# Kernel tuning notes

Hardware: AMD Instinct MI355X
Metric: run time of the kernel (lower is better)

## Reference

```python
import jax, jax.numpy as jnp
import numpy as np

NUM_POINTS = 4_000_000
RADIUS = 2.5
IMG = 1024


def setup_inputs() -> dict:
    key = jax.random.key(0)
    k1, k2, k3, k4 = jax.random.split(key, 4)
    # Uniform sampling inside a sphere, mirroring the torch __init__
    phi = jax.random.uniform(k1, (NUM_POINTS,)) * 2 * np.pi
    costheta = jax.random.uniform(k2, (NUM_POINTS,)) * 2 - 1
    u = jax.random.uniform(k3, (NUM_POINTS,))
    theta = jnp.arccos(costheta)
    r = RADIUS * u ** (1.0 / 3.0)
    x = r * jnp.sin(theta) * jnp.cos(phi)
    y = r * jnp.sin(theta) * jnp.sin(phi)
    z = r * jnp.cos(theta)
    positions = jnp.stack([x, y, z], axis=-1).astype(jnp.float32)  # [N,3]
    colors = jax.random.uniform(k4, (NUM_POINTS, 3), dtype=jnp.float32)
    # Camera at origin looking down +z, points translated to z in [2.5, 7.5]
    camera_pose = jnp.eye(4, dtype=jnp.float32).at[2, 3].set(5.0)
    intrinsics = jnp.array([[800.0, 0.0, 512.0],
                            [0.0, 800.0, 512.0],
                            [0.0, 0.0, 1.0]], dtype=jnp.float32)
    return {"positions": positions, "colors": colors,
            "camera_pose": camera_pose, "intrinsics": intrinsics,
            "H": IMG, "W": IMG}


def reference(positions, colors, camera_pose, intrinsics, H, W):
    # points_cam = (R @ P^T)^T + t^T
    R = camera_pose[:3, :3]
    t = camera_pose[:3, 3]
    pc = positions @ R.T + t  # [N,3]
    x, y, z = pc[:, 0], pc[:, 1], pc[:, 2]
    fx, fy = intrinsics[0, 0], intrinsics[1, 1]
    cx, cy = intrinsics[0, 2], intrinsics[1, 2]
    u = fx * x / z + cx
    v = fy * y / z + cy
    # int() truncation toward zero, matching the torch loop
    xi = u.astype(jnp.int32)
    yi = v.astype(jnp.int32)
    valid = (xi >= 0) & (xi < W) & (yi >= 0) & (yi < H)
    n = positions.shape[0]
    pix = jnp.where(valid, yi * W + xi, H * W)  # invalid -> sentinel segment
    winner = jax.ops.segment_max(jnp.arange(n, dtype=jnp.int32), pix,
                                 num_segments=H * W + 1)[: H * W]
    has = winner >= 0  # empty segments get iinfo(int32).min
    img_flat = jnp.where(has[:, None],
                         colors[jnp.clip(winner, 0, n - 1)],
                         jnp.float32(0.0))  # [H*W, 3]
    img = img_flat.reshape(H, W, 3).transpose(2, 0, 1)[None]  # [1,3,H,W]
    return jnp.clip(img, 0.0, 1.0)
```

## Files before the change

### kernel.cpp

```cpp
#include <hip/hip_runtime.h>


#define NB      1024
#define TB      512
#define TBP     1024
#define NT      1024
#define GP      4
#define NG      (NT / GP)
#define PPB_MAX 4096
#define IMGW    1024
#define IMGHW   (1024 * 1024)

__host__ __device__ __forceinline__ unsigned align8u(unsigned x) {
    return (x + 7u) & ~7u;
}

__global__ void __launch_bounds__(TB)
binsort_kernel(const float* __restrict__ pos,
               const float* __restrict__ pose,
               const float* __restrict__ intr,
               unsigned* __restrict__ bins,
               unsigned* __restrict__ histG,
               int n, int ppb, int region) {
    __shared__ unsigned stash[PPB_MAX];
    __shared__ unsigned h[NT];
    __shared__ unsigned base_[NT];
    __shared__ unsigned cur[NT];
    __shared__ unsigned sc[TB];

    int tid = threadIdx.x;
    for (int t = tid; t < NT; t += TB) h[t] = 0;
    __syncthreads();

    float r00 = pose[0], r01 = pose[1], r02 = pose[2],  t0 = pose[3];
    float r10 = pose[4], r11 = pose[5], r12 = pose[6],  t1 = pose[7];
    float r20 = pose[8], r21 = pose[9], r22 = pose[10], t2 = pose[11];
    float fx = intr[0], cx = intr[2];
    float fy = intr[4], cy = intr[5];

    int start = blockIdx.x * ppb;
    int cnt = min(start + ppb, n) - start;
    if (cnt < 0) cnt = 0;

    const float4* p4 = (const float4*)(pos + (size_t)3 * (size_t)start);
    for (int j4 = tid * 4; j4 < cnt; j4 += TB * 4) {
        int g = j4 >> 2;
        float4 A = p4[3 * g + 0];
        float4 B = p4[3 * g + 1];
        float4 C = p4[3 * g + 2];
        float xs0 = A.x, ys0 = A.y, zs0 = A.z;
        float xs1 = A.w, ys1 = B.x, zs1 = B.y;
        float xs2 = B.z, ys2 = B.w, zs2 = C.x;
        float xs3 = C.y, ys3 = C.z, zs3 = C.w;

        unsigned pv[4];
        #define PROJ(K, PX, PY, PZ)                                          \
        {                                                                    \
            float x = r00 * PX + r01 * PY + r02 * PZ + t0;                   \
            float y = r10 * PX + r11 * PY + r12 * PZ + t1;                   \
            float z = r20 * PX + r21 * PY + r22 * PZ + t2;                   \
            float u = fx * x / z + cx;                                       \
            float v = fy * y / z + cy;                                       \
            int xi = (int)u;                                                 \
            int yi = (int)v;                                                 \
            unsigned p = 0xFFFFFFFFu;                                        \
            if (xi >= 0 && xi < IMGW && yi >= 0 && yi < IMGW) {              \
                p = ((unsigned)yi << 10) | (unsigned)xi;                     \
                int tt = ((yi >> 5) << 5) + (xi >> 5);                       \
                atomicAdd(&h[tt], 1u);                                       \
            }                                                                \
            pv[K] = p;                                                       \
        }
        PROJ(0, xs0, ys0, zs0)
        PROJ(1, xs1, ys1, zs1)
        PROJ(2, xs2, ys2, zs2)
        PROJ(3, xs3, ys3, zs3)
        #undef PROJ

        *(uint4*)&stash[j4] = make_uint4(pv[0], pv[1], pv[2], pv[3]);
    }
    __syncthreads();

    unsigned c0 = h[2 * tid];
    unsigned c1 = h[2 * tid + 1];
    unsigned v = c0 + c1;
    sc[tid] = v;
    __syncthreads();
    for (int off = 1; off < TB; off <<= 1) {
        unsigned add = (tid >= off) ? sc[tid - off] : 0u;
        __syncthreads();
        v += add;
        sc[tid] = v;
        __syncthreads();
    }
    base_[2 * tid]     = v - c0 - c1;
    base_[2 * tid + 1] = v - c1;
    __syncthreads();

    for (int t = tid; t < NT; t += TB) {
        cur[t] = base_[t];
        histG[(size_t)(t >> 2) * (NB * 4) + (blockIdx.x << 2) + (t & 3)] =
            (base_[t] << 16) | h[t];
    }
    __syncthreads();

    unsigned* myRegion = bins + (size_t)blockIdx.x * (size_t)region;
    for (int j = tid; j < cnt; j += TB) {
        unsigned pv = stash[j];
        if (pv == 0xFFFFFFFFu) continue;
        unsigned xi = pv & 1023u, yi = pv >> 10;
        unsigned t  = ((yi >> 5) << 5) + (xi >> 5);
        unsigned lp = ((yi & 31u) << 5) + (xi & 31u);
        unsigned slot = atomicAdd(&cur[t], 1u);
        myRegion[slot] = (lp << 22) | (unsigned)(start + j);
    }
}

__global__ void __launch_bounds__(TBP)
paint_kernel(const unsigned* __restrict__ bins,
             const unsigned* __restrict__ histG,
             const float* __restrict__ colors,
             float* __restrict__ out,
             int region) {
    __shared__ uint4    hgs[NB];
    __shared__ unsigned win[GP * 1024];
    int g = blockIdx.x;
    int tid = threadIdx.x;

    hgs[tid] = ((const uint4*)histG)[((size_t)g << 10) + tid];
    #pragma unroll
    for (int l = tid; l < GP * 1024; l += TBP) win[l] = 0;
    __syncthreads();

    int grp = tid >> 4, lane16 = tid & 15;
    for (int b = grp; b < NB; b += (TBP / 16)) {
        uint4 pk = hgs[b];
        unsigned c0 = pk.x & 0xFFFFu, c1 = pk.y & 0xFFFFu;
        unsigned c2 = pk.z & 0xFFFFu, c3 = pk.w & 0xFFFFu;
        unsigned b01 = c0 + c1, b012 = b01 + c2;
        unsigned total = b012 + c3;
        const unsigned* p = bins + (size_t)b * (size_t)region + (pk.x >> 16);
        for (unsigned k = lane16; k < total; k += 16) {
            unsigned e = p[k];
            unsigned s = (k >= c0) + (k >= b01) + (k >= b012);
            atomicMax(&win[(s << 10) + (e >> 22)], (e & 0x3FFFFFu) + 1u);
        }
    }
    __syncthreads();

    int tx0 = ((g * GP) & 31) << 5;
    int ty0 = ((g * GP) >> 5) << 5;
    for (int l = tid; l < GP * 1024; l += TBP) {
        int lx = l & 127, ly = l >> 7;
        int s = lx >> 5, col = lx & 31;
        unsigned w = win[(s << 10) + (ly << 5) + col];
        float r = 0.0f, gc = 0.0f, bl = 0.0f;
        if (w) {
            unsigned wi = w - 1u;
            r  = fminf(fmaxf(colors[3 * wi + 0], 0.0f), 1.0f);
            gc = fminf(fmaxf(colors[3 * wi + 1], 0.0f), 1.0f);
            bl = fminf(fmaxf(colors[3 * wi + 2], 0.0f), 1.0f);
        }
        int p = (ty0 + ly) * IMGW + tx0 + lx;
        out[p] = r;
        out[IMGHW + p] = gc;
        out[2 * IMGHW + p] = bl;
    }
}


__global__ void proj_simple(const float* __restrict__ pos,
                            const float* __restrict__ pose,
                            const float* __restrict__ intr,
                            const int* __restrict__ Hp,
                            const int* __restrict__ Wp,
                            int* __restrict__ winner, int n) {
    int i = blockIdx.x * blockDim.x + threadIdx.x;
    if (i >= n) return;
    float px = pos[3 * i], py = pos[3 * i + 1], pz = pos[3 * i + 2];
    float x = pose[0] * px + pose[1] * py + pose[2]  * pz + pose[3];
    float y = pose[4] * px + pose[5] * py + pose[6]  * pz + pose[7];
    float z = pose[8] * px + pose[9] * py + pose[10] * pz + pose[11];
    float u = intr[0] * x / z + intr[2];
    float v = intr[4] * y / z + intr[5];
    int xi = (int)u, yi = (int)v;
    int W = *Wp, H = *Hp;
    if (xi >= 0 && xi < W && yi >= 0 && yi < H) atomicMax(&winner[yi * W + xi], i);
}

__global__ void paint_simple(const int* __restrict__ winner,
                             const float* __restrict__ colors,
                             float* __restrict__ out, int HW) {
    int p = blockIdx.x * blockDim.x + threadIdx.x;
    if (p >= HW) return;
    int w = winner[p];
    float r = 0.0f, g = 0.0f, b = 0.0f;
    if (w >= 0) {
        r = fminf(fmaxf(colors[3 * w + 0], 0.0f), 1.0f);
        g = fminf(fmaxf(colors[3 * w + 1], 0.0f), 1.0f);
        b = fminf(fmaxf(colors[3 * w + 2], 0.0f), 1.0f);
    }
    out[p] = r; out[HW + p] = g; out[2 * HW + p] = b;
}

extern "C" void kernel_launch(void* const* d_in, const int* in_sizes, int n_in,
                              void* d_out, int out_size, void* d_ws, size_t ws_size,
                              hipStream_t stream) {
    const float* positions = (const float*)d_in[0];
    const float* colors    = (const float*)d_in[1];
    const float* pose      = (const float*)d_in[2];
    const float* intr      = (const float*)d_in[3];
    const int*   Hp        = (const int*)d_in[4];
    const int*   Wp        = (const int*)d_in[5];
    float* out = (float*)d_out;

    int n  = in_sizes[0] / 3;
    int HW = out_size / 3;

    int ppb = ((n + NB - 1) / NB + 3) & ~3;
    int region = (int)align8u((unsigned)ppb);
    unsigned* bins  = (unsigned*)d_ws;
    unsigned* histG = bins + (size_t)NB * (size_t)region;
    size_t needFast = ((size_t)NB * region + (size_t)NB * NT) * sizeof(unsigned);

    bool fast = (HW == IMGHW) && (n >= 4096) && ((n & 3) == 0) &&
                (ppb <= PPB_MAX) && (n <= 4000000) && (ws_size >= needFast);

    if (fast) {
        binsort_kernel<<<NB, TB, 0, stream>>>(positions, pose, intr,
                                              bins, histG, n, ppb, region);
        paint_kernel<<<NG, TBP, 0, stream>>>(bins, histG, colors, out, region);
        return;
    }

    int* winner = (int*)d_ws;
    const int block = 256;
    hipMemsetAsync(winner, 0xFF, (size_t)HW * sizeof(int), stream);
    int grid = (n + block - 1) / block;
    proj_simple<<<grid, block, 0, stream>>>(positions, pose, intr, Hp, Wp,
                                            winner, n);
    int grid2 = (HW + block - 1) / block;
    paint_simple<<<grid2, block, 0, stream>>>(winner, colors, out, HW);
}
```

Baseline: 64.66 us.

## Split paint pass across source-bin slices and add merge-gather kernel

The paint kernel is split so each of the 256 pixel groups is handled by 4 blocks, each covering a quarter of the source bins. Each block writes its partial per-pixel winner indices to a workspace buffer. A new merge kernel takes the max across the 4 partials and gathers the colors. The aim is to raise parallelism from 256 large blocks to 1024 smaller ones so the paint phase fills the GPU better, at the cost of an extra 16 MB partial write and read plus one more kernel launch.

```diff
diff --git a/kernel.cpp b/kernel.cpp
--- a/kernel.cpp
+++ b/kernel.cpp
@@ -3,10 +3,11 @@
 
 #define NB      1024
 #define TB      512
-#define TBP     1024
 #define NT      1024
 #define GP      4
 #define NG      (NT / GP)
+#define RS      4
+#define TPP     256
 #define PPB_MAX 4096
 #define IMGW    1024
 #define IMGHW   (1024 * 1024)
@@ -116,56 +117,69 @@
     }
 }
 
-__global__ void __launch_bounds__(TBP)
-paint_kernel(const unsigned* __restrict__ bins,
-             const unsigned* __restrict__ histG,
-             const float* __restrict__ colors,
-             float* __restrict__ out,
-             int region) {
-    __shared__ uint4    hgs[NB];
+__global__ void __launch_bounds__(TPP)
+paint_partial_kernel(const unsigned* __restrict__ bins,
+                     const unsigned* __restrict__ histG,
+                     unsigned* __restrict__ winpart,
+                     int region) {
+    __shared__ uint4    hgs[NB / RS];
     __shared__ unsigned win[GP * 1024];
-    int g = blockIdx.x;
+    int g = blockIdx.x & (NG - 1);
+    int s = blockIdx.x >> 8;
     int tid = threadIdx.x;
 
-    hgs[tid] = ((const uint4*)histG)[((size_t)g << 10) + tid];
+    hgs[tid] = ((const uint4*)histG)[((size_t)g << 10) + (s << 8) + tid];
     #pragma unroll
-    for (int l = tid; l < GP * 1024; l += TBP) win[l] = 0;
+    for (int l = tid; l < GP * 1024; l += TPP) win[l] = 0;
     __syncthreads();
 
     int grp = tid >> 4, lane16 = tid & 15;
-    for (int b = grp; b < NB; b += (TBP / 16)) {
-        uint4 pk = hgs[b];
+    for (int bl = grp; bl < NB / RS; bl += (TPP / 16)) {
+        uint4 pk = hgs[bl];
         unsigned c0 = pk.x & 0xFFFFu, c1 = pk.y & 0xFFFFu;
         unsigned c2 = pk.z & 0xFFFFu, c3 = pk.w & 0xFFFFu;
         unsigned b01 = c0 + c1, b012 = b01 + c2;
         unsigned total = b012 + c3;
+        int b = (s << 8) + bl;
         const unsigned* p = bins + (size_t)b * (size_t)region + (pk.x >> 16);
         for (unsigned k = lane16; k < total; k += 16) {
             unsigned e = p[k];
-            unsigned s = (k >= c0) + (k >= b01) + (k >= b012);
-            atomicMax(&win[(s << 10) + (e >> 22)], (e & 0x3FFFFFu) + 1u);
+            unsigned st = (k >= c0) + (k >= b01) + (k >= b012);
+            atomicMax(&win[(st << 10) + (e >> 22)], (e & 0x3FFFFFu) + 1u);
         }
     }
     __syncthreads();
 
     int tx0 = ((g * GP) & 31) << 5;
     int ty0 = ((g * GP) >> 5) << 5;
-    for (int l = tid; l < GP * 1024; l += TBP) {
+    unsigned* wp = winpart + (size_t)s * IMGHW;
+    for (int l = tid; l < GP * 1024; l += TPP) {
         int lx = l & 127, ly = l >> 7;
-        int s = lx >> 5, col = lx & 31;
-        unsigned w = win[(s << 10) + (ly << 5) + col];
-        float r = 0.0f, gc = 0.0f, bl = 0.0f;
-        if (w) {
-            unsigned wi = w - 1u;
-            r  = fminf(fmaxf(colors[3 * wi + 0], 0.0f), 1.0f);
-            gc = fminf(fmaxf(colors[3 * wi + 1], 0.0f), 1.0f);
-            bl = fminf(fmaxf(colors[3 * wi + 2], 0.0f), 1.0f);
-        }
-        int p = (ty0 + ly) * IMGW + tx0 + lx;
-        out[p] = r;
-        out[IMGHW + p] = gc;
-        out[2 * IMGHW + p] = bl;
-    }
+        int sb = lx >> 5, col = lx & 31;
+        wp[(ty0 + ly) * IMGW + tx0 + lx] = win[(sb << 10) + (ly << 5) + col];
+    }
+}
+
+__global__ void __launch_bounds__(256)
+merge_gather_kernel(const unsigned* __restrict__ winpart,
+                    const float* __restrict__ colors,
+                    float* __restrict__ out) {
+    int p = blockIdx.x * blockDim.x + threadIdx.x;
+    if (p >= IMGHW) return;
+    unsigned w = winpart[p];
+    w = max(w, winpart[IMGHW + p]);
+    w = max(w, winpart[2 * IMGHW + p]);
+    w = max(w, winpart[3 * IMGHW + p]);
+    float r = 0.0f, g = 0.0f, b = 0.0f;
+    if (w) {
+        unsigned wi = w - 1u;
+        r = fminf(fmaxf(colors[3 * wi + 0], 0.0f), 1.0f);
+        g = fminf(fmaxf(colors[3 * wi + 1], 0.0f), 1.0f);
+        b = fminf(fmaxf(colors[3 * wi + 2], 0.0f), 1.0f);
+    }
+    out[p] = r;
+    out[IMGHW + p] = g;
+    out[2 * IMGHW + p] = b;
 }
 
 
@@ -219,9 +233,11 @@
 
     int ppb = ((n + NB - 1) / NB + 3) & ~3;
     int region = (int)align8u((unsigned)ppb);
-    unsigned* bins  = (unsigned*)d_ws;
-    unsigned* histG = bins + (size_t)NB * (size_t)region;
-    size_t needFast = ((size_t)NB * region + (size_t)NB * NT) * sizeof(unsigned);
+    unsigned* bins    = (unsigned*)d_ws;
+    unsigned* histG   = bins + (size_t)NB * (size_t)region;
+    unsigned* winpart = histG + (size_t)NB * NT;
+    size_t needFast = ((size_t)NB * region + (size_t)NB * NT +
+                       (size_t)RS * IMGHW) * sizeof(unsigned);
 
     bool fast = (HW == IMGHW) && (n >= 4096) && ((n & 3) == 0) &&
                 (ppb <= PPB_MAX) && (n <= 4000000) && (ws_size >= needFast);
@@ -229,7 +245,10 @@
     if (fast) {
         binsort_kernel<<<NB, TB, 0, stream>>>(positions, pose, intr,
                                               bins, histG, n, ppb, region);
-        paint_kernel<<<NG, TBP, 0, stream>>>(bins, histG, colors, out, region);
+        paint_partial_kernel<<<NG * RS, TPP, 0, stream>>>(bins, histG,
+                                                          winpart, region);
+        merge_gather_kernel<<<(IMGHW + 255) / 256, 256, 0, stream>>>(
+            winpart, colors, out);
         return;
     }
 
```

Result: slower. 74.34 us (+15.0%).
